# Optimization experiments

Measured on AMD Instinct MI355X. Metric: run time of the kernel, lower is better.

## Reference

```python
import jax, jax.numpy as jnp
import numpy as np
from jax import lax

B, S, D, NH, K = 4, 2048, 1024, 16, 3
EPS = 1e-6


def custom_layernorm(x, gamma, beta):
    # torch-style: std with ddof=1, eps added to std (not var)
    mean = jnp.mean(x, axis=-1, keepdims=True)
    var = jnp.sum((x - mean) ** 2, axis=-1, keepdims=True) / (x.shape[-1] - 1)
    std = jnp.sqrt(var)
    return gamma * ((x - mean) / (std + EPS)) + beta


def setup_inputs() -> dict:
    key = jax.random.key(0)
    ks = jax.random.split(key, 10)
    s = 1.0 / np.sqrt(D)
    return {
        "x": jax.random.normal(ks[0], (B, S, D), jnp.float32),
        "Wq": jax.random.normal(ks[1], (D, D), jnp.float32) * s,
        "bq": jax.random.normal(ks[2], (D,), jnp.float32) * 0.02,
        "Wk": jax.random.normal(ks[3], (D, D), jnp.float32) * s,
        "Wv": jax.random.normal(ks[4], (D, D), jnp.float32) * s,
        "bv": jax.random.normal(ks[5], (D,), jnp.float32) * 0.02,
        "conv_w": jax.random.normal(ks[6], (D, D // NH, K), jnp.float32) * (1.0 / np.sqrt((D // NH) * K)),
        "conv_b": jax.random.normal(ks[7], (D,), jnp.float32) * 0.02,
        "gamma": jnp.ones((D,), jnp.float32),
        "beta": jnp.zeros((D,), jnp.float32),
        "Wo": jax.random.normal(ks[8], (D, D), jnp.float32) * s,
        "bo": jax.random.normal(ks[9], (D,), jnp.float32) * 0.02,
    }


def reference(x, Wq, bq, Wk, Wv, bv, conv_w, conv_b, gamma, beta, Wo, bo):
    d = x.shape[-1]
    groups = d // conv_w.shape[1]
    pad = conv_w.shape[2] // 2

    q = x @ Wq + bq
    k = x @ Wk  # key has no bias
    v = x @ Wv + bv

    # grouped conv1d over sequence dim (NCW layout)
    xc = jnp.transpose(x, (0, 2, 1))  # [B, D, S]
    conv_out = lax.conv_general_dilated(
        xc, conv_w, window_strides=(1,), padding=[(pad, pad)],
        feature_group_count=groups,
        dimension_numbers=("NCH", "OIH", "NCH"),
    ) + conv_b[None, :, None]
    conv_out = jnp.transpose(conv_out, (0, 2, 1))  # [B, S, D]
    conv_out = custom_layernorm(conv_out, gamma, beta)  # dropout = identity (eval)

    scale = 1.0 / jnp.sqrt(jnp.asarray(d, x.dtype))
    scores = jnp.einsum("bqd,bkd->bqk", q, k) * scale  # [B, S, S]
    attn = jax.nn.softmax(scores, axis=-1)
    attention_out = jnp.einsum("bqk,bkd->bqd", attn, v)

    combined = custom_layernorm(conv_out + attention_out, gamma, beta)
    return combined @ Wo + bo + x
```

## Files before the change

kernel.cpp:

```cpp
#include <hip/hip_runtime.h>
#include <cstdint>


#define DEV __device__ __forceinline__

typedef unsigned short u16;
typedef __attribute__((ext_vector_type(8))) short bf16x8;
typedef __attribute__((ext_vector_type(4))) float f32x4;

static const int Sn = 2048, Dn = 1024;

DEV float bf2f(u16 u) { union { unsigned int i; float f; } w; w.i = ((unsigned int)u) << 16; return w.f; }
DEV u16 f2bf(float f) {
  union { float f; unsigned int i; } w; w.f = f;
  unsigned int x = w.i;
  return (u16)((x + 0x7FFFu + ((x >> 16) & 1u)) >> 16);
}

DEV void gload_lds16(const u16* gsrc, u16* lds_dst) {
  __builtin_amdgcn_global_load_lds(
      (const __attribute__((address_space(1))) void*)gsrc,
      (__attribute__((address_space(3))) void*)lds_dst,
      16, 0, 0);
}

DEV float block_allreduce_sum(float v, float* red, int tid) {
  #pragma unroll
  for (int o = 32; o > 0; o >>= 1) v += __shfl_down(v, o, 64);
  __syncthreads();
  if ((tid & 63) == 0) red[tid >> 6] = v;
  __syncthreads();
  return red[0] + red[1] + red[2] + red[3];
}

DEV float block_allreduce_max(float v, float* red, int tid) {
  #pragma unroll
  for (int o = 32; o > 0; o >>= 1) v = fmaxf(v, __shfl_down(v, o, 64));
  __syncthreads();
  if ((tid & 63) == 0) red[tid >> 6] = v;
  __syncthreads();
  return fmaxf(fmaxf(red[0], red[1]), fmaxf(red[2], red[3]));
}

DEV void ln_row(const u16* __restrict__ a, const u16* __restrict__ b2,
                const float* __restrict__ gamma, const float* __restrict__ beta,
                u16* __restrict__ out, long row, int tid, float* red) {
  long base = row * Dn + tid * 4;
  ushort4 av = *(const ushort4*)&a[base];
  float v0 = bf2f(av.x), v1 = bf2f(av.y), v2 = bf2f(av.z), v3 = bf2f(av.w);
  if (b2) {
    ushort4 bv4 = *(const ushort4*)&b2[base];
    v0 += bf2f(bv4.x); v1 += bf2f(bv4.y); v2 += bf2f(bv4.z); v3 += bf2f(bv4.w);
  }
  float s = block_allreduce_sum(v0 + v1 + v2 + v3, red, tid);
  float mean = s * (1.0f / 1024.0f);
  float d0 = v0 - mean, d1 = v1 - mean, d2 = v2 - mean, d3 = v3 - mean;
  float sq = block_allreduce_sum(d0 * d0 + d1 * d1 + d2 * d2 + d3 * d3, red, tid);
  float inv = 1.0f / (sqrtf(sq * (1.0f / 1023.0f)) + 1e-6f);
  float4 gv = *(const float4*)&gamma[tid * 4];
  float4 bev = *(const float4*)&beta[tid * 4];
  ushort4 o;
  o.x = f2bf(gv.x * d0 * inv + bev.x);
  o.y = f2bf(gv.y * d1 * inv + bev.y);
  o.z = f2bf(gv.z * d2 * inv + bev.z);
  o.w = f2bf(gv.w * d3 * inv + bev.w);
  *(ushort4*)&out[base] = o;
}

__global__ __launch_bounds__(256)
void prep_all(const float* __restrict__ Wq, const float* __restrict__ Wk,
              const float* __restrict__ Wv, const float* __restrict__ Wo,
              u16* __restrict__ wT,
              const float* __restrict__ bq, const float* __restrict__ bv,
              float* __restrict__ qkvb,
              const float* __restrict__ x, u16* __restrict__ xb) {
  __shared__ u16 sm[64][68];
  int blk = blockIdx.x;
  int tid = threadIdx.x;
  if (blk < 1024) {
    int w = blk >> 8, t = blk & 255;
    const float* src = (w == 0) ? Wq : (w == 1) ? Wk : (w == 2) ? Wv : Wo;
    u16* dst = wT + (size_t)w * 1048576u;
    int i0 = (t >> 4) << 6, j0 = (t & 15) << 6;
    int tx = tid & 15, r0 = tid >> 4;
    #pragma unroll
    for (int rr = r0; rr < 64; rr += 16) {
      float4 v = *(const float4*)&src[(long)(i0 + rr) * 1024 + j0 + tx * 4];
      sm[rr][tx*4+0] = f2bf(v.x); sm[rr][tx*4+1] = f2bf(v.y);
      sm[rr][tx*4+2] = f2bf(v.z); sm[rr][tx*4+3] = f2bf(v.w);
    }
    __syncthreads();
    #pragma unroll
    for (int cc = r0; cc < 64; cc += 16) {
      ushort4 o;
      o.x = sm[tx*4+0][cc]; o.y = sm[tx*4+1][cc];
      o.z = sm[tx*4+2][cc]; o.w = sm[tx*4+3][cc];
      *(ushort4*)&dst[(long)(j0 + cc) * 1024 + i0 + tx * 4] = o;
    }
  } else if (blk == 1024) {
    for (int j = tid; j < 3072; j += 256) {
      float v = 0.0f;
      if (j < 1024) v = bq[j];
      else if (j >= 2048) v = bv[j - 2048];
      qkvb[j] = v;
    }
  } else {
    int i = (blk - 1025) * 1024 + tid * 4;
    float4 v = *(const float4*)&x[i];
    ushort4 o;
    o.x = f2bf(v.x); o.y = f2bf(v.y); o.z = f2bf(v.z); o.w = f2bf(v.w);
    *(ushort4*)&xb[i] = o;
  }
}

__global__ __launch_bounds__(512, 2)
void gemm8(const u16* __restrict__ A, long Abs, int lda,
           const u16* __restrict__ B, long Bbs, int ldb,
           u16* __restrict__ C0, u16* __restrict__ C1, int zsplit,
           long Cbs, int ldc, int K, float scale,
           const float* __restrict__ bias, int bias_bs) {
  extern __shared__ ulong2 lds_raw[];
  u16* lds = (u16*)lds_raw;
  int tid = threadIdx.x;
  int w = tid >> 6, ln = tid & 63;
  int quad = ln >> 4, lm = ln & 15;
  int wr = w >> 2, wc = w & 3;
  long m0 = (long)blockIdx.x * 256, n0 = (long)blockIdx.y * 256;
  int z = blockIdx.z;
  A += (long)z * Abs;
  B += (long)z * Bbs;
  u16* C = (z < zsplit) ? C0 + (long)z * Cbs : C1 + (long)(z - zsplit) * Cbs;

  int sg = ((ln & 7) ^ (ln >> 3)) * 8;
  int row0 = w * 8 + (ln >> 3);
  const u16* As0 = A + (m0 + row0) * (long)lda + sg;
  const u16* As1 = As0 + 64 * (long)lda;
  const u16* Bs0 = B + (n0 + row0) * (long)ldb + sg;
  const u16* Bs1 = Bs0 + 64 * (long)ldb;
  u16* dA = lds + w * 512;
  u16* dB = lds + 16384 + w * 512;

  int rA = wr * 16 + lm;
  int rB = wc * 16 + lm;
  int g0 = (quad ^ (lm & 7)) * 8;
  int g1 = ((4 + quad) ^ (lm & 7)) * 8;

#define STGA(buf, h, k0) do { \
    gload_lds16(As0 + (long)(h) * 128 * lda + (k0), dA + (buf) * 32768 + (h) * 8192); \
    gload_lds16(As1 + (long)(h) * 128 * lda + (k0), dA + (buf) * 32768 + (h) * 8192 + 4096); } while (0)
#define STGB(buf, h, k0) do { \
    gload_lds16(Bs0 + (long)(h) * 128 * ldb + (k0), dB + (buf) * 32768 + (h) * 8192); \
    gload_lds16(Bs1 + (long)(h) * 128 * ldb + (k0), dB + (buf) * 32768 + (h) * 8192 + 4096); } while (0)
#define LDA_F(ab, mi, kk) (*(const bf16x8*)&lds[(ab) + ((mi) * 32 + rA) * 64 + ((kk) ? g1 : g0)])
#define LDB_F(bb, ni, kk) (*(const bf16x8*)&lds[(bb) + ((ni) * 64 + rB) * 64 + ((kk) ? g1 : g0)])
#define MFMA(a, b, c) __builtin_amdgcn_mfma_f32_16x16x32_bf16(a, b, c, 0, 0, 0)
#define CLUSTER(S, MLO, MHI) do { \
    _Pragma("unroll") \
    for (int ni = 0; ni < 4; ni++) { \
      acc[MLO][ni] = MFMA(bfr[ni][0], S[0], acc[MLO][ni]); \
      acc[MLO][ni] = MFMA(bfr[ni][1], S[1], acc[MLO][ni]); \
      acc[MHI][ni] = MFMA(bfr[ni][0], S[2], acc[MHI][ni]); \
      acc[MHI][ni] = MFMA(bfr[ni][1], S[3], acc[MHI][ni]); \
    } } while (0)
#define RDA(dst, base, mi) do { \
    dst[0] = LDA_F(base, mi, 0); dst[1] = LDA_F(base, mi, 1); \
    dst[2] = LDA_F(base, (mi) + 1, 0); dst[3] = LDA_F(base, (mi) + 1, 1); } while (0)
#define VMCNT(n) do { asm volatile("s_waitcnt vmcnt(" #n ")" ::: "memory"); \
    __builtin_amdgcn_sched_barrier(0); } while (0)
#define BAR() __builtin_amdgcn_s_barrier()

  f32x4 acc[8][4] = {};
  bf16x8 bfr[4][2];
  bf16x8 nb0[2], nb1[2];
  bf16x8 aE[4], aO[4];
  int nt = K >> 6;

  STGA(0, 0, 0); STGB(0, 0, 0); STGB(0, 1, 0); STGA(0, 1, 0);
  VMCNT(4);
  BAR();
  {
    RDA(aE, 0, 0);
    bfr[0][0] = LDB_F(16384, 0, 0); bfr[0][1] = LDB_F(16384, 0, 1);
    bfr[1][0] = LDB_F(16384, 1, 0); bfr[1][1] = LDB_F(16384, 1, 1);
  }
  VMCNT(2);
  BAR();

  for (int t = 0; t < nt; ++t) {
    int buf = t & 1;
    int abase = buf * 32768, bbase = abase + 16384;
    int nbuf = buf ^ 1;
    int nbabase = nbuf * 32768, nbbbase = nbabase + 16384;
    int kn = (t + 1) << 6;
    bool more = (t + 1 < nt);

    bfr[2][0] = LDB_F(bbase, 2, 0); bfr[2][1] = LDB_F(bbase, 2, 1);
    bfr[3][0] = LDB_F(bbase, 3, 0); bfr[3][1] = LDB_F(bbase, 3, 1);
    RDA(aO, abase, 2);
    if (more) STGA(nbuf, 0, kn);
    BAR();
    __builtin_amdgcn_s_setprio(1);
    CLUSTER(aE, 0, 1);
    __builtin_amdgcn_s_setprio(0);
    if (more) VMCNT(2); else VMCNT(0);
    BAR();
    RDA(aE, abase, 4);
    if (more) STGB(nbuf, 0, kn);
    BAR();
    __builtin_amdgcn_s_setprio(1);
    CLUSTER(aO, 2, 3);
    __builtin_amdgcn_s_setprio(0);
    BAR();
    RDA(aO, abase, 6);
    if (more) STGB(nbuf, 1, kn);
    BAR();
    __builtin_amdgcn_s_setprio(1);
    CLUSTER(aE, 4, 5);
    __builtin_amdgcn_s_setprio(0);
    if (more) VMCNT(2);
    BAR();
    if (more) {
      RDA(aE, nbabase, 0);
      nb0[0] = LDB_F(nbbbase, 0, 0); nb0[1] = LDB_F(nbbbase, 0, 1);
      nb1[0] = LDB_F(nbbbase, 1, 0); nb1[1] = LDB_F(nbbbase, 1, 1);
      STGA(nbuf, 1, kn);
    }
    BAR();
    __builtin_amdgcn_s_setprio(1);
    CLUSTER(aO, 6, 7);
    __builtin_amdgcn_s_setprio(0);
    if (more) VMCNT(2);
    BAR();
    if (more) {
      bfr[0][0] = nb0[0]; bfr[0][1] = nb0[1];
      bfr[1][0] = nb1[0]; bfr[1][1] = nb1[1];
    }
  }

  #pragma unroll
  for (int mi = 0; mi < 8; mi++) {
    long m = m0 + mi * 32 + wr * 16 + lm;
    u16* Crow = C + m * (long)ldc;
    #pragma unroll
    for (int ni = 0; ni < 4; ni++) {
      int nb = (int)n0 + ni * 64 + wc * 16 + quad * 4;
      float4 bv4;
      if (bias) bv4 = *(const float4*)&bias[(long)z * bias_bs + nb];
      else      bv4 = float4{0.0f, 0.0f, 0.0f, 0.0f};
      ushort4 o;
      o.x = f2bf(acc[mi][ni][0] * scale + bv4.x);
      o.y = f2bf(acc[mi][ni][1] * scale + bv4.y);
      o.z = f2bf(acc[mi][ni][2] * scale + bv4.z);
      o.w = f2bf(acc[mi][ni][3] * scale + bv4.w);
      *(ushort4*)&Crow[nb] = o;
    }
  }
#undef STGA
#undef STGB
#undef LDA_F
#undef LDB_F
#undef MFMA
#undef CLUSTER
#undef RDA
#undef VMCNT
#undef BAR
}

template<typename CT>
__global__ __launch_bounds__(256, 2)
void gemm_nt(const u16* __restrict__ A, const u16* __restrict__ A2, long Abs, int lda,
             const u16* __restrict__ B, long Bbs, int ldb,
             CT* __restrict__ C, CT* __restrict__ C2, long Cbs, int ldc,
             int zsplit, int K, float scale,
             const float* __restrict__ bias, int bias_bs,
             const float* __restrict__ res, long Rbs, int ldr) {
  __shared__ u16 sA[2][128 * 32];
  __shared__ u16 sB[2][128 * 32];
  int tid = threadIdx.x;
  int lane = tid & 63, wv = tid >> 6;
  int quad = lane >> 4, lm = lane & 15;
  int wr = wv >> 1, wc = wv & 1;
  long m0 = (long)blockIdx.x * 128, n0 = (long)blockIdx.y * 128;
  int z = blockIdx.z;
  if (z >= zsplit) { A = A2 + (long)(z - zsplit) * Abs; C = C2 + (long)(z - zsplit) * Cbs; }
  else             { A = A  + (long)z * Abs;            C = C  + (long)z * Cbs; }
  B += (long)z * Bbs;
  if (res) res += (long)z * Rbs;

  f32x4 acc[4][4] = {};

  int srow = wv * 16 + (lane >> 2);
  int sch = (lane & 3) * 8;
  const u16* Ap = A + (m0 + srow) * (long)lda + sch;
  const u16* Bp = B + (n0 + srow) * (long)ldb + sch;
  const int lofs = wv * 16 * 32;

  for (int k0 = 0; k0 < K; k0 += 64) {
    #pragma unroll
    for (int h = 0; h < 2; h++) {
      int kh = k0 + h * 32;
      gload_lds16(Ap + kh, &sA[h][lofs]);
      gload_lds16(Ap + 64 * (long)lda + kh, &sA[h][lofs + 64 * 32]);
      gload_lds16(Bp + kh, &sB[h][lofs]);
      gload_lds16(Bp + 64 * (long)ldb + kh, &sB[h][lofs + 64 * 32]);
    }
    __syncthreads();
    #pragma unroll
    for (int h = 0; h < 2; h++) {
      bf16x8 af[4], bfr[4];
      #pragma unroll
      for (int mi = 0; mi < 4; mi++)
        af[mi] = *(const bf16x8*)&sA[h][(wr * 64 + mi * 16 + lm) * 32 + quad * 8];
      #pragma unroll
      for (int ni = 0; ni < 4; ni++)
        bfr[ni] = *(const bf16x8*)&sB[h][(wc * 64 + ni * 16 + lm) * 32 + quad * 8];
      #pragma unroll
      for (int mi = 0; mi < 4; mi++)
        #pragma unroll
        for (int ni = 0; ni < 4; ni++)
          acc[mi][ni] = __builtin_amdgcn_mfma_f32_16x16x32_bf16(af[mi], bfr[ni], acc[mi][ni], 0, 0, 0);
    }
    __syncthreads();
  }

  #pragma unroll
  for (int mi = 0; mi < 4; mi++) {
    #pragma unroll
    for (int ni = 0; ni < 4; ni++) {
      int col = (int)n0 + wc * 64 + ni * 16 + lm;
      float bv = bias ? bias[(long)z * bias_bs + col] : 0.0f;
      #pragma unroll
      for (int r = 0; r < 4; r++) {
        long rowg = m0 + wr * 64 + mi * 16 + quad * 4 + r;
        float v = acc[mi][ni][r] * scale + bv;
        if (res) v += res[rowg * (long)ldr + col];
        if constexpr (sizeof(CT) == 2) C[rowg * (long)ldc + col] = f2bf(v);
        else                           C[rowg * (long)ldc + col] = v;
      }
    }
  }
}

__global__ __launch_bounds__(256, 2)
void post_qkv(int ngemm,
              const u16* __restrict__ Qb, const u16* __restrict__ Kb,
              u16* __restrict__ Pd, u16* __restrict__ Pw,
              const u16* __restrict__ Vb, u16* __restrict__ vt) {
  __shared__ u16 smem[2 * 2 * 128 * 32];
  int blk = blockIdx.x;
  int tid = threadIdx.x;
  if (blk < ngemm) {
    u16* sA0 = smem;
    u16* sB0 = smem + 2 * 128 * 32;
    int lane = tid & 63, wv = tid >> 6;
    int quad = lane >> 4, lm = lane & 15;
    int wr = wv >> 1, wc = wv & 1;
    int z = blk >> 8;
    long m0 = (long)(blk & 15) * 128, n0 = (long)((blk >> 4) & 15) * 128;
    const u16* A = Qb + (long)z * Sn * Dn;
    const u16* B = Kb + (long)z * Sn * Dn;
    u16* C = (z < 2) ? Pd + (long)z * Sn * Sn : Pw + (long)(z - 2) * Sn * Sn;

    f32x4 acc[4][4] = {};
    int srow = wv * 16 + (lane >> 2);
    int sch = (lane & 3) * 8;
    const u16* Ap = A + (m0 + srow) * 1024 + sch;
    const u16* Bp = B + (n0 + srow) * 1024 + sch;
    const int lofs = wv * 16 * 32;

    for (int k0 = 0; k0 < 1024; k0 += 64) {
      #pragma unroll
      for (int h = 0; h < 2; h++) {
        int kh = k0 + h * 32;
        gload_lds16(Ap + kh, &sA0[h * 128 * 32 + lofs]);
        gload_lds16(Ap + 64 * 1024 + kh, &sA0[h * 128 * 32 + lofs + 64 * 32]);
        gload_lds16(Bp + kh, &sB0[h * 128 * 32 + lofs]);
        gload_lds16(Bp + 64 * 1024 + kh, &sB0[h * 128 * 32 + lofs + 64 * 32]);
      }
      __syncthreads();
      #pragma unroll
      for (int h = 0; h < 2; h++) {
        bf16x8 af[4], bfr[4];
        #pragma unroll
        for (int mi = 0; mi < 4; mi++)
          af[mi] = *(const bf16x8*)&sA0[h * 128 * 32 + (wr * 64 + mi * 16 + lm) * 32 + quad * 8];
        #pragma unroll
        for (int ni = 0; ni < 4; ni++)
          bfr[ni] = *(const bf16x8*)&sB0[h * 128 * 32 + (wc * 64 + ni * 16 + lm) * 32 + quad * 8];
        #pragma unroll
        for (int mi = 0; mi < 4; mi++)
          #pragma unroll
          for (int ni = 0; ni < 4; ni++)
            acc[mi][ni] = __builtin_amdgcn_mfma_f32_16x16x32_bf16(af[mi], bfr[ni], acc[mi][ni], 0, 0, 0);
      }
      __syncthreads();
    }
    #pragma unroll
    for (int mi = 0; mi < 4; mi++) {
      #pragma unroll
      for (int ni = 0; ni < 4; ni++) {
        int col = (int)n0 + wc * 64 + ni * 16 + lm;
        #pragma unroll
        for (int r = 0; r < 4; r++) {
          long rowg = m0 + wr * 64 + mi * 16 + quad * 4 + r;
          C[rowg * 2048 + col] = f2bf(acc[mi][ni][r] * 0.03125f);
        }
      }
    }
  } else {
    u16 (*sm)[68] = (u16(*)[68])smem;
    int t = blk - ngemm;
    int b = t >> 9, r = t & 511;
    int j0 = (r & 15) << 6, i0 = ((r >> 4) & 31) << 6;
    const u16* s = Vb + (long)b * Sn * Dn;
    u16* d = vt + (long)b * Dn * Sn;
    int tx = tid & 15, r0 = tid >> 4;
    #pragma unroll
    for (int rr = r0; rr < 64; rr += 16) {
      ushort4 v = *(const ushort4*)&s[(long)(i0 + rr) * 1024 + j0 + tx * 4];
      sm[rr][tx*4+0] = v.x; sm[rr][tx*4+1] = v.y; sm[rr][tx*4+2] = v.z; sm[rr][tx*4+3] = v.w;
    }
    __syncthreads();
    #pragma unroll
    for (int cc = r0; cc < 64; cc += 16) {
      ushort4 o;
      o.x = sm[tx*4+0][cc]; o.y = sm[tx*4+1][cc];
      o.z = sm[tx*4+2][cc]; o.w = sm[tx*4+3][cc];
      *(ushort4*)&d[(long)(j0 + cc) * 2048 + i0 + tx * 4] = o;
    }
  }
}

__global__ __launch_bounds__(256)
void smax_conv(u16* __restrict__ pa, u16* __restrict__ pb, int rowsplit,
               int nsm, int nconv,
               const float* __restrict__ x, const float* __restrict__ cw,
               const float* __restrict__ cb, u16* __restrict__ convo,
               const u16* __restrict__ Vb, u16* __restrict__ vt) {
  __shared__ u16 smem[22160];
  __shared__ float red[4];
  int blk = blockIdx.x;
  int tid = threadIdx.x;
  if (blk < nsm) {
    long row = blk;
    u16* p = (row < rowsplit) ? pa + row * 2048 : pb + (row - rowsplit) * 2048;
    ushort4 a = *(const ushort4*)&p[tid * 8];
    ushort4 b = *(const ushort4*)&p[tid * 8 + 4];
    float f0 = bf2f(a.x), f1 = bf2f(a.y), f2 = bf2f(a.z), f3 = bf2f(a.w);
    float f4 = bf2f(b.x), f5 = bf2f(b.y), f6 = bf2f(b.z), f7 = bf2f(b.w);
    float m = fmaxf(fmaxf(fmaxf(f0, f1), fmaxf(f2, f3)),
                    fmaxf(fmaxf(f4, f5), fmaxf(f6, f7)));
    m = block_allreduce_max(m, red, tid);
    float e0 = __expf(f0 - m), e1 = __expf(f1 - m), e2 = __expf(f2 - m), e3 = __expf(f3 - m);
    float e4 = __expf(f4 - m), e5 = __expf(f5 - m), e6 = __expf(f6 - m), e7 = __expf(f7 - m);
    float s = block_allreduce_sum(e0 + e1 + e2 + e3 + e4 + e5 + e6 + e7, red, tid);
    float inv = 1.0f / s;
    ushort4 o1, o2;
    o1.x = f2bf(e0 * inv); o1.y = f2bf(e1 * inv); o1.z = f2bf(e2 * inv); o1.w = f2bf(e3 * inv);
    o2.x = f2bf(e4 * inv); o2.y = f2bf(e5 * inv); o2.z = f2bf(e6 * inv); o2.w = f2bf(e7 * inv);
    *(ushort4*)&p[tid * 8] = o1;
    *(ushort4*)&p[tid * 8 + 4] = o2;
  } else if (blk < nsm + nconv) {
    u16 (*sx)[72] = (u16(*)[72])smem;
    u16 (*sw)[200] = (u16(*)[200])(smem + 9360);
    int r = blk - nsm;
    int s0 = (r & 15) * 128;
    int g = (r >> 4) & 15;
    int b = r >> 8;
    int lane = tid & 63, wv = tid >> 6;
    int quad = lane >> 4, lm = lane & 15;
    for (int idx = tid; idx < 64 * 192; idx += 256) {
      int oc = idx / 192, k = idx - oc * 192;
      int t = k >> 6, i = k & 63;
      sw[oc][k] = f2bf(cw[((long)(g * 64 + oc)) * 192 + i * 3 + t]);
    }
    for (int idx = tid; idx < 130 * 16; idx += 256) {
      int rr = idx >> 4, c4 = (idx & 15) * 4;
      int s = s0 - 1 + rr;
      ushort4 v;
      if (s >= 0 && s < Sn) {
        float4 f = *(const float4*)&x[((long)b * Sn + s) * Dn + g * 64 + c4];
        v.x = f2bf(f.x); v.y = f2bf(f.y); v.z = f2bf(f.z); v.w = f2bf(f.w);
      } else { v.x = 0; v.y = 0; v.z = 0; v.w = 0; }
      *(ushort4*)&sx[rr][c4] = v;
    }
    __syncthreads();
    f32x4 acc[2][4] = {};
    #pragma unroll
    for (int ks = 0; ks < 6; ks++) {
      int t = ks >> 1;
      int i0 = (ks & 1) * 32 + quad * 8;
      bf16x8 a0 = *(const bf16x8*)&sx[wv * 32 + lm + t][i0];
      bf16x8 a1 = *(const bf16x8*)&sx[wv * 32 + 16 + lm + t][i0];
      #pragma unroll
      for (int nf = 0; nf < 4; nf++) {
        bf16x8 bf = *(const bf16x8*)&sw[nf * 16 + lm][ks * 32 + quad * 8];
        acc[0][nf] = __builtin_amdgcn_mfma_f32_16x16x32_bf16(a0, bf, acc[0][nf], 0, 0, 0);
        acc[1][nf] = __builtin_amdgcn_mfma_f32_16x16x32_bf16(a1, bf, acc[1][nf], 0, 0, 0);
      }
    }
    #pragma unroll
    for (int mi = 0; mi < 2; mi++) {
      #pragma unroll
      for (int nf = 0; nf < 4; nf++) {
        int col = g * 64 + nf * 16 + lm;
        float bias = cb[col];
        #pragma unroll
        for (int rr = 0; rr < 4; rr++) {
          int row = wv * 32 + mi * 16 + quad * 4 + rr;
          convo[((long)b * Sn + s0 + row) * Dn + col] = f2bf(acc[mi][nf][rr] + bias);
        }
      }
    }
  } else {
    u16 (*sm)[68] = (u16(*)[68])smem;
    int t = blk - nsm - nconv;
    int b = t >> 9, r = t & 511;
    int j0 = (r & 15) << 6, i0 = ((r >> 4) & 31) << 6;
    const u16* s = Vb + (long)b * Sn * Dn;
    u16* d = vt + (long)b * Dn * Sn;
    int tx = tid & 15, r0 = tid >> 4;
    #pragma unroll
    for (int rr = r0; rr < 64; rr += 16) {
      ushort4 v = *(const ushort4*)&s[(long)(i0 + rr) * 1024 + j0 + tx * 4];
      sm[rr][tx*4+0] = v.x; sm[rr][tx*4+1] = v.y; sm[rr][tx*4+2] = v.z; sm[rr][tx*4+3] = v.w;
    }
    __syncthreads();
    #pragma unroll
    for (int cc = r0; cc < 64; cc += 16) {
      ushort4 o;
      o.x = sm[tx*4+0][cc]; o.y = sm[tx*4+1][cc];
      o.z = sm[tx*4+2][cc]; o.w = sm[tx*4+3][cc];
      *(ushort4*)&d[(long)(j0 + cc) * 2048 + i0 + tx * 4] = o;
    }
  }
}

__global__ __launch_bounds__(256, 2)
void pv_ln(int npv,
           const u16* __restrict__ Pd, const u16* __restrict__ Pw,
           const u16* __restrict__ vt, u16* __restrict__ attn,
           u16* __restrict__ conv,
           const float* __restrict__ gamma, const float* __restrict__ beta) {
  __shared__ u16 smem[2 * 2 * 128 * 32];
  __shared__ float red[4];
  int blk = blockIdx.x;
  int tid = threadIdx.x;
  if (blk < npv) {
    u16* sA0 = smem;
    u16* sB0 = smem + 2 * 128 * 32;
    int lane = tid & 63, wv = tid >> 6;
    int quad = lane >> 4, lm = lane & 15;
    int wr = wv >> 1, wc = wv & 1;
    int z = blk >> 7;
    long m0 = (long)(blk & 15) * 128, n0 = (long)((blk >> 4) & 7) * 128;
    const u16* A = (z < 2) ? Pd + (long)z * Sn * Sn : Pw + (long)(z - 2) * Sn * Sn;
    const u16* B = vt + (long)z * Dn * Sn;
    u16* C = attn + (long)z * Sn * Dn;

    f32x4 acc[4][4] = {};
    int srow = wv * 16 + (lane >> 2);
    int sch = (lane & 3) * 8;
    const u16* Ap = A + (m0 + srow) * 2048 + sch;
    const u16* Bp = B + (n0 + srow) * 2048 + sch;
    const int lofs = wv * 16 * 32;

    for (int k0 = 0; k0 < 2048; k0 += 64) {
      #pragma unroll
      for (int h = 0; h < 2; h++) {
        int kh = k0 + h * 32;
        gload_lds16(Ap + kh, &sA0[h * 128 * 32 + lofs]);
        gload_lds16(Ap + 64 * 2048 + kh, &sA0[h * 128 * 32 + lofs + 64 * 32]);
        gload_lds16(Bp + kh, &sB0[h * 128 * 32 + lofs]);
        gload_lds16(Bp + 64 * 2048 + kh, &sB0[h * 128 * 32 + lofs + 64 * 32]);
      }
      __syncthreads();
      #pragma unroll
      for (int h = 0; h < 2; h++) {
        bf16x8 af[4], bfr[4];
        #pragma unroll
        for (int mi = 0; mi < 4; mi++)
          af[mi] = *(const bf16x8*)&sA0[h * 128 * 32 + (wr * 64 + mi * 16 + lm) * 32 + quad * 8];
        #pragma unroll
        for (int ni = 0; ni < 4; ni++)
          bfr[ni] = *(const bf16x8*)&sB0[h * 128 * 32 + (wc * 64 + ni * 16 + lm) * 32 + quad * 8];
        #pragma unroll
        for (int mi = 0; mi < 4; mi++)
          #pragma unroll
          for (int ni = 0; ni < 4; ni++)
            acc[mi][ni] = __builtin_amdgcn_mfma_f32_16x16x32_bf16(af[mi], bfr[ni], acc[mi][ni], 0, 0, 0);
      }
      __syncthreads();
    }
    #pragma unroll
    for (int mi = 0; mi < 4; mi++) {
      #pragma unroll
      for (int ni = 0; ni < 4; ni++) {
        int col = (int)n0 + wc * 64 + ni * 16 + lm;
        #pragma unroll
        for (int r = 0; r < 4; r++) {
          long rowg = m0 + wr * 64 + mi * 16 + quad * 4 + r;
          C[rowg * 1024 + col] = f2bf(acc[mi][ni][r]);
        }
      }
    }
  } else {
    long row = blk - npv;
    ln_row(conv, nullptr, gamma, beta, conv, row, tid, red);
  }
}

__global__ __launch_bounds__(256)
void ln_kernel(const u16* __restrict__ a, const u16* __restrict__ b2,
               const float* __restrict__ gamma, const float* __restrict__ beta,
               u16* __restrict__ out) {
  __shared__ float red[4];
  ln_row(a, b2, gamma, beta, out, blockIdx.x, threadIdx.x, red);
}

static const size_t OFF_WT    = 0;
static const size_t OFF_QKVB  = 8ull << 20;
static const size_t OFF_Q     = 9ull << 20;
static const size_t OFF_K     = 25ull << 20;
static const size_t OFF_V     = 41ull << 20;
static const size_t OFF_PW    = 57ull << 20;

extern "C" void kernel_launch(void* const* d_in, const int* in_sizes, int n_in,
                              void* d_out, int out_size, void* d_ws, size_t ws_size,
                              hipStream_t stream) {
  const float* x     = (const float*)d_in[0];
  const float* Wq    = (const float*)d_in[1];
  const float* bq    = (const float*)d_in[2];
  const float* Wk    = (const float*)d_in[3];
  const float* Wv    = (const float*)d_in[4];
  const float* bv    = (const float*)d_in[5];
  const float* cw    = (const float*)d_in[6];
  const float* cb    = (const float*)d_in[7];
  const float* gamma = (const float*)d_in[8];
  const float* beta  = (const float*)d_in[9];
  const float* Wo    = (const float*)d_in[10];
  const float* bo    = (const float*)d_in[11];
  float* out = (float*)d_out;
  char* ws = (char*)d_ws;

  u16*   wT    = (u16*)(ws + OFF_WT);
  float* qkvb  = (float*)(ws + OFF_QKVB);
  u16*   Qb    = (u16*)(ws + OFF_Q);
  u16*   Kb    = (u16*)(ws + OFF_K);
  u16*   Vb    = (u16*)(ws + OFF_V);
  u16*   Pw    = (u16*)(ws + OFF_PW);
  u16*   xb    = (u16*)d_out;
  u16*   Pd    = (u16*)d_out;
  u16*   vt    = (u16*)d_out + 8388608;
  u16*   attn  = Qb;
  u16*   combined = Kb;
  const long PBS = (long)Sn * Sn;

  static int gemm8_attr = 0;
  if (!gemm8_attr) {
    hipFuncSetAttribute((const void*)gemm8,
                        hipFuncAttributeMaxDynamicSharedMemorySize, 131072);
    gemm8_attr = 1;
  }

  dim3 tb(256);
  dim3 tb8(512);

  prep_all<<<dim3(9217), tb, 0, stream>>>(Wq, Wk, Wv, Wo, wT, bq, bv, qkvb, x, xb);
  gemm8<<<dim3(32, 4, 3), tb8, 131072, stream>>>(
      xb, 0, 1024, wT, 1048576, 1024,
      Qb, (u16*)nullptr, 99, 8388608, 1024,
      1024, 1.0f, qkvb, 1024);

  if (ws_size >= (73ull << 20)) {
    u16* conv = Kb;
    gemm8<<<dim3(8, 8, 4), tb8, 131072, stream>>>(
        Qb, (long)Sn * Dn, 1024, Kb, (long)Sn * Dn, 1024,
        Pd, Pw, 2, PBS, 2048,
        1024, 0.03125f, nullptr, 0);
    smax_conv<<<dim3(8192 + 1024 + 2048), tb, 0, stream>>>(
        Pd, Pw, 4096, 8192, 1024, x, cw, cb, conv, Vb, vt);
    pv_ln<<<dim3(512 + 8192), tb, 0, stream>>>(512, Pd, Pw, vt, attn, conv,
                                               gamma, beta);
    ln_kernel<<<dim3(8192), tb, 0, stream>>>(conv, attn, gamma, beta, combined);
  } else {
    u16* conv = Vb;
    post_qkv<<<dim3(2048), tb, 0, stream>>>(0, Qb, Kb, Pd, Pw, Vb, vt);
    for (int c = 0; c < 2; c++) {
      long off = (long)c * 2 * Sn * Dn;
      gemm_nt<u16><<<dim3(16, 16, 2), tb, 0, stream>>>(
          Qb + off, nullptr, (long)Sn * Dn, 1024, Kb + off, (long)Sn * Dn, 1024,
          Pd, (u16*)nullptr, PBS, 2048,
          99, 1024, 0.03125f, nullptr, 0, nullptr, 0, 0);
      smax_conv<<<dim3(4096 + (c == 0 ? 1024 : 0)), tb, 0, stream>>>(
          Pd, Pd, 4096, 4096, (c == 0 ? 1024 : 0), x, cw, cb, conv, Vb, vt);
      gemm_nt<u16><<<dim3(16, 8, 2), tb, 0, stream>>>(
          Pd, nullptr, PBS, 2048, vt + off, (long)Dn * Sn, 2048,
          attn + off, (u16*)nullptr, (long)Sn * Dn, 1024,
          99, 2048, 1.0f, nullptr, 0, nullptr, 0, 0);
    }
    ln_kernel<<<dim3(8192), tb, 0, stream>>>(conv, nullptr, gamma, beta, conv);
    ln_kernel<<<dim3(8192), tb, 0, stream>>>(conv, attn, gamma, beta, combined);
  }

  gemm_nt<float><<<dim3(64, 8, 1), tb, 0, stream>>>(
      combined, nullptr, 0, 1024, wT + 3u * 1048576u, 0, 1024,
      out, (float*)nullptr, 0, 1024,
      99, 1024, 1.0f, bo, 0, x, 0, 1024);
}
```

Baseline: 374.6 us.

## Simplify GEMM main loop to issue all next-tile loads upfront, no register prefetch

Replaces the staggered 8-wave-style schedule, which interleaved global-to-LDS stages with MFMA clusters and prefetched next-tile fragments into registers, with a simpler loop. The new loop loads all B fragments per tile, issues every next-tile global_load_lds at the start, and reads A fragments just before each cluster. This reduces register pressure and schedule complexity but lowers overlap between LDS reads and MFMAs. The VMCNT thresholds are changed to match the new load ordering.

```diff
diff --git a/kernel.cpp b/kernel.cpp
--- a/kernel.cpp
+++ b/kernel.cpp
@@ -154,86 +154,76 @@
 #define LDA_F(ab, mi, kk) (*(const bf16x8*)&lds[(ab) + ((mi) * 32 + rA) * 64 + ((kk) ? g1 : g0)])
 #define LDB_F(bb, ni, kk) (*(const bf16x8*)&lds[(bb) + ((ni) * 64 + rB) * 64 + ((kk) ? g1 : g0)])
 #define MFMA(a, b, c) __builtin_amdgcn_mfma_f32_16x16x32_bf16(a, b, c, 0, 0, 0)
-#define CLUSTER(S, MLO, MHI) do { \
+#define CLUSTER(A00, A01, A10, A11, MLO, MHI) do { \
     _Pragma("unroll") \
     for (int ni = 0; ni < 4; ni++) { \
-      acc[MLO][ni] = MFMA(bfr[ni][0], S[0], acc[MLO][ni]); \
-      acc[MLO][ni] = MFMA(bfr[ni][1], S[1], acc[MLO][ni]); \
-      acc[MHI][ni] = MFMA(bfr[ni][0], S[2], acc[MHI][ni]); \
-      acc[MHI][ni] = MFMA(bfr[ni][1], S[3], acc[MHI][ni]); \
+      acc[MLO][ni] = MFMA(bfr[ni][0], A00, acc[MLO][ni]); \
+      acc[MLO][ni] = MFMA(bfr[ni][1], A01, acc[MLO][ni]); \
+      acc[MHI][ni] = MFMA(bfr[ni][0], A10, acc[MHI][ni]); \
+      acc[MHI][ni] = MFMA(bfr[ni][1], A11, acc[MHI][ni]); \
     } } while (0)
-#define RDA(dst, base, mi) do { \
-    dst[0] = LDA_F(base, mi, 0); dst[1] = LDA_F(base, mi, 1); \
-    dst[2] = LDA_F(base, (mi) + 1, 0); dst[3] = LDA_F(base, (mi) + 1, 1); } while (0)
 #define VMCNT(n) do { asm volatile("s_waitcnt vmcnt(" #n ")" ::: "memory"); \
     __builtin_amdgcn_sched_barrier(0); } while (0)
 #define BAR() __builtin_amdgcn_s_barrier()
 
   f32x4 acc[8][4] = {};
   bf16x8 bfr[4][2];
-  bf16x8 nb0[2], nb1[2];
-  bf16x8 aE[4], aO[4];
   int nt = K >> 6;
 
   STGA(0, 0, 0); STGB(0, 0, 0); STGB(0, 1, 0); STGA(0, 1, 0);
-  VMCNT(4);
-  BAR();
-  {
-    RDA(aE, 0, 0);
-    bfr[0][0] = LDB_F(16384, 0, 0); bfr[0][1] = LDB_F(16384, 0, 1);
-    bfr[1][0] = LDB_F(16384, 1, 0); bfr[1][1] = LDB_F(16384, 1, 1);
-  }
-  VMCNT(2);
+  VMCNT(0);
   BAR();
 
   for (int t = 0; t < nt; ++t) {
     int buf = t & 1;
     int abase = buf * 32768, bbase = abase + 16384;
     int nbuf = buf ^ 1;
-    int nbabase = nbuf * 32768, nbbbase = nbabase + 16384;
     int kn = (t + 1) << 6;
     bool more = (t + 1 < nt);
 
-    bfr[2][0] = LDB_F(bbase, 2, 0); bfr[2][1] = LDB_F(bbase, 2, 1);
-    bfr[3][0] = LDB_F(bbase, 3, 0); bfr[3][1] = LDB_F(bbase, 3, 1);
-    RDA(aO, abase, 2);
-    if (more) STGA(nbuf, 0, kn);
-    BAR();
-    __builtin_amdgcn_s_setprio(1);
-    CLUSTER(aE, 0, 1);
-    __builtin_amdgcn_s_setprio(0);
-    if (more) VMCNT(2); else VMCNT(0);
-    BAR();
-    RDA(aE, abase, 4);
-    if (more) STGB(nbuf, 0, kn);
-    BAR();
-    __builtin_amdgcn_s_setprio(1);
-    CLUSTER(aO, 2, 3);
-    __builtin_amdgcn_s_setprio(0);
-    BAR();
-    RDA(aO, abase, 6);
-    if (more) STGB(nbuf, 1, kn);
-    BAR();
-    __builtin_amdgcn_s_setprio(1);
-    CLUSTER(aE, 4, 5);
-    __builtin_amdgcn_s_setprio(0);
-    if (more) VMCNT(2);
-    BAR();
-    if (more) {
-      RDA(aE, nbabase, 0);
-      nb0[0] = LDB_F(nbbbase, 0, 0); nb0[1] = LDB_F(nbbbase, 0, 1);
-      nb1[0] = LDB_F(nbbbase, 1, 0); nb1[1] = LDB_F(nbbbase, 1, 1);
-      STGA(nbuf, 1, kn);
-    }
-    BAR();
-    __builtin_amdgcn_s_setprio(1);
-    CLUSTER(aO, 6, 7);
-    __builtin_amdgcn_s_setprio(0);
-    if (more) VMCNT(2);
-    BAR();
-    if (more) {
-      bfr[0][0] = nb0[0]; bfr[0][1] = nb0[1];
-      bfr[1][0] = nb1[0]; bfr[1][1] = nb1[1];
+    {
+      #pragma unroll
+      for (int ni = 0; ni < 4; ni++) {
+        bfr[ni][0] = LDB_F(bbase, ni, 0);
+        bfr[ni][1] = LDB_F(bbase, ni, 1);
+      }
+      bf16x8 a00 = LDA_F(abase, 0, 0), a01 = LDA_F(abase, 0, 1);
+      bf16x8 a10 = LDA_F(abase, 1, 0), a11 = LDA_F(abase, 1, 1);
+      if (more) { STGA(nbuf, 0, kn); STGB(nbuf, 0, kn); STGB(nbuf, 1, kn); STGA(nbuf, 1, kn); }
+      BAR();
+      __builtin_amdgcn_s_setprio(1);
+      CLUSTER(a00, a01, a10, a11, 0, 1);
+      __builtin_amdgcn_s_setprio(0);
+      BAR();
+    }
+    {
+      bf16x8 a00 = LDA_F(abase, 2, 0), a01 = LDA_F(abase, 2, 1);
+      bf16x8 a10 = LDA_F(abase, 3, 0), a11 = LDA_F(abase, 3, 1);
+      BAR();
+      __builtin_amdgcn_s_setprio(1);
+      CLUSTER(a00, a01, a10, a11, 2, 3);
+      __builtin_amdgcn_s_setprio(0);
+      if (more) VMCNT(8); else VMCNT(0);
+      BAR();
+    }
+    {
+      bf16x8 a00 = LDA_F(abase, 4, 0), a01 = LDA_F(abase, 4, 1);
+      bf16x8 a10 = LDA_F(abase, 5, 0), a11 = LDA_F(abase, 5, 1);
+      BAR();
+      __builtin_amdgcn_s_setprio(1);
+      CLUSTER(a00, a01, a10, a11, 4, 5);
+      __builtin_amdgcn_s_setprio(0);
+      BAR();
+    }
+    {
+      bf16x8 a00 = LDA_F(abase, 6, 0), a01 = LDA_F(abase, 6, 1);
+      bf16x8 a10 = LDA_F(abase, 7, 0), a11 = LDA_F(abase, 7, 1);
+      BAR();
+      __builtin_amdgcn_s_setprio(1);
+      CLUSTER(a00, a01, a10, a11, 6, 7);
+      __builtin_amdgcn_s_setprio(0);
+      if (more) VMCNT(2);
+      BAR();
     }
   }
 
@@ -261,7 +251,6 @@
 #undef LDB_F
 #undef MFMA
 #undef CLUSTER
-#undef RDA
 #undef VMCNT
 #undef BAR
 }
```

Result: no change. 372.9 us (-0.5%).
